# Kernel tuning notes

Hardware: AMD Instinct MI355X
Metric: run time of the kernel (lower is better)

Reference implementation:

```python
import jax, jax.numpy as jnp
import numpy as np
import math

B, NRES, RPR = 1, 384, 3
L = NRES * RPR          # 1152 rigids
CS, CZ = 256, 128
CH, H, PQ, PV = 16, 8, 8, 12


def _ln(x, scale, bias):
    mu = jnp.mean(x, axis=-1, keepdims=True)
    var = jnp.var(x, axis=-1, keepdims=True)
    return (x - mu) * jax.lax.rsqrt(var + 1e-5) * scale + bias


def _quat_to_rot(q):
    q = q / jnp.linalg.norm(q, axis=-1, keepdims=True)
    w, x, y, z = q[..., 0], q[..., 1], q[..., 2], q[..., 3]
    r = jnp.stack([
        1 - 2 * (y * y + z * z), 2 * (x * y - w * z), 2 * (x * z + w * y),
        2 * (x * y + w * z), 1 - 2 * (x * x + z * z), 2 * (y * z - w * x),
        2 * (x * z - w * y), 2 * (y * z + w * x), 1 - 2 * (x * x + y * y),
    ], axis=-1)
    return r.reshape(q.shape[:-1] + (3, 3))


def setup_inputs() -> dict:
    key = jax.random.key(0)
    ks = jax.random.split(key, 20)
    s = jax.random.normal(ks[0], (B, L, CS), jnp.float32)
    z = jax.random.normal(ks[1], (B, NRES, NRES, CZ), jnp.float32)
    rot = _quat_to_rot(jax.random.normal(ks[2], (B, L, 4), jnp.float32))
    trans = 10.0 * jax.random.normal(ks[3], (B, L, 3), jnp.float32)
    mask = jnp.ones((B, L), jnp.float32)
    rigid_to_res_idx = jnp.broadcast_to(jnp.arange(L, dtype=jnp.int32) // RPR, (B, L))
    w = lambda k, sh: 0.02 * jax.random.normal(k, sh, jnp.float32)
    return {
        "s": s, "z": z, "rot": rot, "trans": trans, "mask": mask,
        "ln_s_scale": jnp.ones((CS,), jnp.float32), "ln_s_bias": jnp.zeros((CS,), jnp.float32),
        "ln_z_scale": jnp.ones((CZ,), jnp.float32), "ln_z_bias": jnp.zeros((CZ,), jnp.float32),
        "w_q": w(ks[4], (CS, H * CH)), "w_k": w(ks[5], (CS, H * CH)), "w_v": w(ks[6], (CS, H * CH)),
        "w_qp": w(ks[7], (CS, H * PQ * 3)), "w_kp": w(ks[8], (CS, H * PQ * 3)), "w_vp": w(ks[9], (CS, H * PV * 3)),
        "w_b": w(ks[10], (CZ, H)),
        "head_weights": jnp.full((H,), 0.5413, jnp.float32),  # softplus^-1(1)
        "w_out": w(ks[11], (H * (CH + CZ + PV * 4), CS)),
        "b_out": jnp.zeros((CS,), jnp.float32),
        "rigid_to_res_idx": rigid_to_res_idx,
    }


def reference(s, z, rot, trans, mask, ln_s_scale, ln_s_bias, ln_z_scale, ln_z_bias,
              w_q, w_k, w_v, w_qp, w_kp, w_vp, w_b, head_weights, w_out, b_out,
              rigid_to_res_idx):
    b_, l_ = s.shape[0], s.shape[1]
    idx = rigid_to_res_idx[0]                       # [L] rigid -> residue, shared over batch
    s_ln = _ln(s, ln_s_scale, ln_s_bias)            # [B,L,CS]
    z_ln = _ln(z, ln_z_scale, ln_z_bias)            # [B,N,N,CZ]

    q = (s_ln @ w_q).reshape(b_, l_, H, CH)
    k = (s_ln @ w_k).reshape(b_, l_, H, CH)
    v = (s_ln @ w_v).reshape(b_, l_, H, CH)

    # local points, then rigid-transform to global frame: x_g = R x + t
    q_p = (s_ln @ w_qp).reshape(b_, l_, H, PQ, 3)
    k_p = (s_ln @ w_kp).reshape(b_, l_, H, PQ, 3)
    v_p = (s_ln @ w_vp).reshape(b_, l_, H, PV, 3)
    t5 = trans[:, :, None, None, :]
    q_g = jnp.einsum("blij,blhpj->blhpi", rot, q_p) + t5
    k_g = jnp.einsum("blij,blhpj->blhpi", rot, k_p) + t5
    v_g = jnp.einsum("blij,blhpj->blhpi", rot, v_p) + t5

    # scalar qk term
    a = jnp.einsum("blhc,bjhc->bhlj", q, k) * math.sqrt(1.0 / (3 * CH))
    # pair bias, broadcast residue-pair -> rigid-pair
    b_res = z_ln @ w_b                                # [B,N,N,H]
    b_full = b_res[:, idx][:, :, idx]                 # [B,L,L,H]
    a = a + math.sqrt(1.0 / 3) * jnp.transpose(b_full, (0, 3, 1, 2))
    # point-distance term: ||q-k||^2 = |q|^2 + |k|^2 - 2 q.k (summed over P,3)
    hw = jax.nn.softplus(head_weights) * math.sqrt(1.0 / (3 * (PQ * 9.0 / 2)))
    qq = jnp.sum(q_g * q_g, axis=(-1, -2)).transpose(0, 2, 1)   # [B,H,L]
    kk = jnp.sum(k_g * k_g, axis=(-1, -2)).transpose(0, 2, 1)
    qk = jnp.einsum("blhpc,bjhpc->bhlj", q_g, k_g)
    d2 = qq[:, :, :, None] + kk[:, :, None, :] - 2.0 * qk
    a = a - 0.5 * d2 * hw[None, :, None, None]
    a = a + (mask[:, None, None, :] - 1.0) * 1e9
    attn = jax.nn.softmax(a, axis=-1)                 # [B,H,L,L]

    o = jnp.einsum("bhlj,bjhc->blhc", attn, v)        # [B,L,H,CH]
    o_pt_g = jnp.einsum("bhlj,bjhpc->blhpc", attn, v_g)
    # back to local frame of query rigid: R^T (x - t)
    o_pt = jnp.einsum("blji,blhpj->blhpi", rot, o_pt_g - t5)
    o_pt_norm = jnp.sqrt(jnp.sum(o_pt * o_pt, axis=-1) + 1e-8)  # [B,L,H,PV]
    # pair output: sum attention over rigids belonging to each key residue
    attn_res = attn.reshape(b_, H, l_, NRES, RPR).sum(-1)       # [B,H,L,N]
    z_l = z_ln[:, idx]                                           # [B,L,N,CZ]
    o_pair = jnp.einsum("bhln,blnc->blhc", attn_res, z_l)        # [B,L,H,CZ]

    cat = jnp.concatenate(
        [o, o_pt.reshape(b_, l_, H, PV * 3), o_pt_norm, o_pair], axis=-1
    ).reshape(b_, l_, H * (CH + PV * 4 + CZ))
    return cat @ w_out + b_out                        # [B,L,CS]
```

## Files before the change

### kernel.cpp

```cpp
#include <hip/hip_runtime.h>
#include <hip/hip_bf16.h>

#define L 1152
#define NRES 384
#define CS 256
#define CZ 128
#define H 8
#define CH 16
#define PQ 8
#define PV 12
#define PSTR 1088

#define OFF_SLN  0L
#define OFF_PROJ 294912L
#define OFF_WPK  1548288L
#define OFF_QCAT 1826816L
#define OFF_KCAT 2232320L
#define OFF_VCAT 2637824L
#define OFF_BRES 3227648L
#define OFF_MURS 4407296L
#define OFF_ATTN 4702208L
#define OFF_CAT  15319040L
#define OFF_PCAT 17088512L
#define OFF_RSTAT 18268160L
#define OFF_PAV  18286592L
#define OFF_POP  21825536L
#define OFF_ARES 26544128L

__global__ __launch_bounds__(256) void k_ln_s(const float* s, const float* sc, const float* bi, float* sln){
  int l = blockIdx.x, t = threadIdx.x;
  __shared__ float red[CS];
  float x = s[(long)l*CS + t];
  red[t] = x; __syncthreads();
  for(int st=128; st>0; st>>=1){ if(t<st) red[t]+=red[t+st]; __syncthreads(); }
  float mu = red[0] * (1.f/CS); __syncthreads();
  float d = x - mu;
  red[t] = d*d; __syncthreads();
  for(int st=128; st>0; st>>=1){ if(t<st) red[t]+=red[t+st]; __syncthreads(); }
  float var = red[0]*(1.f/CS);
  sln[(long)l*CS + t] = d*rsqrtf(var + 1e-5f)*sc[t] + bi[t];
}

__global__ __launch_bounds__(256) void k_packw(const float* wq, const float* wk, const float* wv,
                        const float* wqp, const float* wkp, const float* wvp, float* wpack){
  int k = blockIdx.x, t = threadIdx.x;
  for(int c=t; c<PSTR; c+=256){
    float v;
    if(c<128)        v = wq [(long)k*128 + c];
    else if(c<256)   v = wk [(long)k*128 + c-128];
    else if(c<384)   v = wv [(long)k*128 + c-256];
    else if(c<576)   v = wqp[(long)k*192 + c-384];
    else if(c<768)   v = wkp[(long)k*192 + c-576];
    else if(c<1056)  v = wvp[(long)k*288 + c-768];
    else             v = 0.f;
    wpack[(long)k*PSTR + c] = v;
  }
}

__global__ __launch_bounds__(256) void k_proj(const float* sln, const float* wpack, float* proj){
  int l0 = blockIdx.x*64, c0 = blockIdx.y*64, t = threadIdx.x;
  __shared__ float a_s[32][68];
  __shared__ __align__(16) float w_s[32][68];
  int tr = t>>4, tc = t&15;
  float4 acc[4] = {{0,0,0,0},{0,0,0,0},{0,0,0,0},{0,0,0,0}};
  for(int kc=0; kc<8; kc++){
    int k0 = kc*32;
    {
      int row = t>>2, kk0 = (t&3)*8;
      const float4* src = (const float4*)(sln + (long)(l0+row)*256 + k0 + kk0);
      float4 v0 = src[0], v1 = src[1];
      a_s[kk0+0][row]=v0.x; a_s[kk0+1][row]=v0.y; a_s[kk0+2][row]=v0.z; a_s[kk0+3][row]=v0.w;
      a_s[kk0+4][row]=v1.x; a_s[kk0+5][row]=v1.y; a_s[kk0+6][row]=v1.z; a_s[kk0+7][row]=v1.w;
    }
    #pragma unroll
    for(int kk2=0; kk2<2; kk2++){
      int kk = (t>>4) + 16*kk2;
      *(float4*)&w_s[kk][(t&15)*4] = *(const float4*)(wpack + (long)(k0+kk)*PSTR + c0 + (t&15)*4);
    }
    __syncthreads();
    #pragma unroll 8
    for(int kk=0; kk<32; kk++){
      float4 a4 = *(const float4*)&a_s[kk][tr*4];
      float4 b4 = *(const float4*)&w_s[kk][tc*4];
      acc[0].x+=a4.x*b4.x; acc[0].y+=a4.x*b4.y; acc[0].z+=a4.x*b4.z; acc[0].w+=a4.x*b4.w;
      acc[1].x+=a4.y*b4.x; acc[1].y+=a4.y*b4.y; acc[1].z+=a4.y*b4.z; acc[1].w+=a4.y*b4.w;
      acc[2].x+=a4.z*b4.x; acc[2].y+=a4.z*b4.y; acc[2].z+=a4.z*b4.z; acc[2].w+=a4.z*b4.w;
      acc[3].x+=a4.w*b4.x; acc[3].y+=a4.w*b4.y; acc[3].z+=a4.w*b4.z; acc[3].w+=a4.w*b4.w;
    }
    __syncthreads();
  }
  #pragma unroll
  for(int r=0;r<4;r++)
    *(float4*)(proj + (long)(l0 + tr*4 + r)*PSTR + c0 + tc*4) = acc[r];
}

__global__ __launch_bounds__(256) void k_ln_z(const float* z, const float* sc, const float* bi,
                       const float* wb, float* murs, float* bres_t){
  int t = threadIdx.x;
  long rp0 = (long)blockIdx.x*32;
  int r = t>>3, part = t&7;
  long rp = rp0 + r;
  __shared__ __align__(16) float swb[8*132];
  __shared__ float SB[8][2];
  const float4* z4 = (const float4*)z;
  float4 x0 = z4[rp*32 + part*4 + 0];
  float4 x1 = z4[rp*32 + part*4 + 1];
  float4 x2 = z4[rp*32 + part*4 + 2];
  float4 x3 = z4[rp*32 + part*4 + 3];
  #pragma unroll
  for(int k2=0;k2<4;k2++){
    int e = t + k2*256; int h = e>>7, c = e&127;
    swb[h*132 + c] = sc[c]*wb[(long)c*8 + h];
  }
  __syncthreads();
  if(t < 64){
    int h = t>>3, seg = t&7;
    float S=0, Bv=0;
    #pragma unroll
    for(int i=0;i<16;i++){
      int c = seg*16+i;
      S  += swb[h*132+c];
      Bv += bi[c]*wb[(long)c*8 + h];
    }
    #pragma unroll
    for(int off=1;off<8;off<<=1){ S += __shfl_xor(S,off,64); Bv += __shfl_xor(Bv,off,64); }
    if(seg==0){ SB[h][0]=S; SB[h][1]=Bv; }
  }
  float s1 = x0.x+x0.y+x0.z+x0.w + x1.x+x1.y+x1.z+x1.w
           + x2.x+x2.y+x2.z+x2.w + x3.x+x3.y+x3.z+x3.w;
  float s2 = x0.x*x0.x+x0.y*x0.y+x0.z*x0.z+x0.w*x0.w
           + x1.x*x1.x+x1.y*x1.y+x1.z*x1.z+x1.w*x1.w
           + x2.x*x2.x+x2.y*x2.y+x2.z*x2.z+x2.w*x2.w
           + x3.x*x3.x+x3.y*x3.y+x3.z*x3.z+x3.w*x3.w;
  #pragma unroll
  for(int off=1;off<8;off<<=1){ s1 += __shfl_xor(s1,off,64); s2 += __shfl_xor(s2,off,64); }
  float mu = s1*(1.f/CZ);
  float var = s2*(1.f/CZ) - mu*mu;
  float rstd = rsqrtf(var + 1e-5f);
  if(part==0){ murs[rp*2]=mu; murs[rp*2+1]=rstd; }
  float acc[8];
  const float4* swb4 = (const float4*)swb;
  #pragma unroll
  for(int h=0;h<8;h++){
    float4 wa = swb4[h*33 + part*4 + 0];
    float4 wbv= swb4[h*33 + part*4 + 1];
    float4 wc = swb4[h*33 + part*4 + 2];
    float4 wd = swb4[h*33 + part*4 + 3];
    acc[h] = x0.x*wa.x + x0.y*wa.y + x0.z*wa.z + x0.w*wa.w
           + x1.x*wbv.x+ x1.y*wbv.y+ x1.z*wbv.z+ x1.w*wbv.w
           + x2.x*wc.x + x2.y*wc.y + x2.z*wc.z + x2.w*wc.w
           + x3.x*wd.x + x3.y*wd.y + x3.z*wd.z + x3.w*wd.w;
  }
  #pragma unroll
  for(int off=1;off<8;off<<=1){
    #pragma unroll
    for(int h=0;h<8;h++) acc[h] += __shfl_xor(acc[h],off,64);
  }
  __syncthreads();
  if(part==0){
    #pragma unroll
    for(int h=0;h<8;h++)
      bres_t[(long)h*147456 + rp] = rstd*(acc[h] - mu*SB[h][0]) + SB[h][1];
  }
}

__global__ __launch_bounds__(256) void k_rigid(const float* proj, const float* rot, const float* trans,
                        const float* mask, const float* hws,
                        float* qcat, float* kcat, float* vcat){
  int l = blockIdx.x, t = threadIdx.x;
  __shared__ float R[9], T[3], hwS[8], qgs[192], kgs[192];
  if(t<9) R[t]=rot[(long)l*9+t];
  if(t<3) T[t]=trans[(long)l*3+t];
  if(t>=16 && t<24) hwS[t-16] = log1pf(expf(hws[t-16]))*0.09622504486493764f;
  __syncthreads();
  const float* pr = proj + (long)l*PSTR;
  if(t<128){
    int h=t>>4, c=t&15;
    long base = ((long)h*L + l)*44;
    qcat[base + c] = 0.14433756729740643f * pr[t];
    kcat[base + c] = pr[128+t];
    vcat[((long)h*L + l)*64 + c] = pr[256+t];
  }
  if(t < 192){
    int h=t/24, m=t%24, p=m/3, i=m%3;
    float qa = R[i*3+0]*pr[384+h*24+p*3+0] + R[i*3+1]*pr[384+h*24+p*3+1]
             + R[i*3+2]*pr[384+h*24+p*3+2] + T[i];
    float ka = R[i*3+0]*pr[576+h*24+p*3+0] + R[i*3+1]*pr[576+h*24+p*3+1]
             + R[i*3+2]*pr[576+h*24+p*3+2] + T[i];
    qgs[t]=qa; kgs[t]=ka;
    long base = ((long)h*L + l)*44 + 16 + m;
    qcat[base] = hwS[h]*qa;
    kcat[base] = ka;
  }
  for(int it=t; it<288; it+=256){
    int h=it/36, m=it%36, p=m/3, i=m%3;
    float a = R[i*3+0]*pr[768+h*36+p*3+0] + R[i*3+1]*pr[768+h*36+p*3+1]
            + R[i*3+2]*pr[768+h*36+p*3+2] + T[i];
    vcat[((long)h*L + l)*64 + 16 + m] = a;
  }
  if(t < 96){
    int h=t/12, d=t%12;
    vcat[((long)h*L + l)*64 + 52 + d] = 0.f;
  }
  __syncthreads();
  if(t < 8){
    float qq=0, kk=0;
    #pragma unroll
    for(int m=0;m<24;m++){ qq += qgs[t*24+m]*qgs[t*24+m]; kk += kgs[t*24+m]*kgs[t*24+m]; }
    long base = ((long)t*L + l)*44;
    qcat[base + 40] = -0.5f*hwS[t]*qq;
    kcat[base + 40] = -0.5f*hwS[t]*kk + (mask[l]-1.f)*1e9f;
  }
}

__global__ __launch_bounds__(256) void k_scores(const float* qcat, const float* kcat,
                         const float* bres_t, const int* ridx, float* attn){
  int l0 = blockIdx.x*32, j0 = blockIdx.y*64, h = blockIdx.z;
  int t = threadIdx.x;
  __shared__ __align__(16) float q_s[32*44];
  __shared__ __align__(16) float k_s[64*44];
  __shared__ int rj_s[64];
  {
    const float* srcq = qcat + ((long)h*L + l0)*44;
    for(int i=t; i<32*44; i+=256) q_s[i]=srcq[i];
    const float* srck = kcat + ((long)h*L + j0)*44;
    for(int i=t; i<64*44; i+=256) k_s[i]=srck[i];
    if(t<64) rj_s[t]=ridx[j0+t];
  }
  __syncthreads();
  int a = t>>5;
  int b = t&31;
  float acc[4][2] = {{0,0},{0,0},{0,0},{0,0}};
  const float4* q4 = (const float4*)q_s;
  const float4* k4 = (const float4*)k_s;
  #pragma unroll
  for(int i=0;i<10;i++){
    float4 kA = k4[(long)b*11 + i];
    float4 kB = k4[(long)(b+32)*11 + i];
    #pragma unroll
    for(int r=0;r<4;r++){
      float4 qv = q4[(long)(a+8*r)*11 + i];
      acc[r][0] += qv.x*kA.x + qv.y*kA.y + qv.z*kA.z + qv.w*kA.w;
      acc[r][1] += qv.x*kB.x + qv.y*kB.y + qv.z*kB.z + qv.w*kB.w;
    }
  }
  float colc0 = k_s[b*44+40], colc1 = k_s[(b+32)*44+40];
  int rj0 = rj_s[b], rj1 = rj_s[b+32];
  const float* bbh = bres_t + (long)h*147456;
  #pragma unroll
  for(int r=0;r<4;r++){
    int row = a+8*r;
    float rowc = q_s[row*44+40];
    int rl = ridx[l0+row];
    const float* bb = bbh + (long)rl*NRES;
    float s0 = acc[r][0] + rowc + colc0 + 0.5773502691896258f*bb[rj0];
    float s1 = acc[r][1] + rowc + colc1 + 0.5773502691896258f*bb[rj1];
    float* arow = attn + ((long)h*L + l0+row)*L + j0;
    arow[b]    = s0;
    arow[b+32] = s1;
  }
}

__global__ __launch_bounds__(256) void k_rowstat(const float* attn, float* rowstat, float* ares){
  long row = (long)blockIdx.x*4 + (threadIdx.x>>6);
  int lane = threadIdx.x & 63;
  int w = threadIdx.x >> 6;
  __shared__ float es[4][1152];
  const float* p = attn + row*L;
  float v[18];
  float m=-1e30f;
  #pragma unroll
  for(int i=0;i<18;i++){ v[i]=p[lane + i*64]; m=fmaxf(m,v[i]); }
  #pragma unroll
  for(int off=1;off<64;off<<=1) m=fmaxf(m,__shfl_xor(m,off,64));
  float s=0;
  #pragma unroll
  for(int i=0;i<18;i++){ v[i]=__expf(v[i]-m); s+=v[i]; }
  #pragma unroll
  for(int off=1;off<64;off<<=1) s+=__shfl_xor(s,off,64);
  float inv = 1.f/s;
  if(lane==0){ rowstat[row*2]=m; rowstat[row*2+1]=inv; }
  #pragma unroll
  for(int i=0;i<18;i++) es[w][lane + i*64] = v[i]*inv;
  __syncthreads();
  #pragma unroll
  for(int q=0;q<6;q++){
    int n = lane + q*64;
    ares[row*NRES + n] = es[w][3*n] + es[w][3*n+1] + es[w][3*n+2];
  }
}

__global__ __launch_bounds__(256) void k_av(const float* attn, const float* vcat,
                     const float* rowstat, float* pav){
  int lb = blockIdx.x, h = blockIdx.y, sp = blockIdx.z, t = threadIdx.x;
  int l0 = lb*32;
  __shared__ float a_s[64][33];
  __shared__ __align__(16) float v_s[64][68];
  int lgrp = t>>4, dgrp = t&15;
  float4 acc0 = {0,0,0,0}, acc1 = {0,0,0,0};
  const float* abase = attn + ((long)h*L + l0)*L;
  int al = t>>3, jj0 = (t&7)*8;
  float mrow = rowstat[((long)h*L + l0 + al)*2];
  float irow = rowstat[((long)h*L + l0 + al)*2 + 1];
  for(int jc=sp*3; jc<sp*3+3; jc++){
    int j0 = jc*64;
    {
      const float4* src = (const float4*)(abase + (long)al*L + j0 + jj0);
      float4 p0 = src[0], p1 = src[1];
      a_s[jj0+0][al]=__expf(p0.x-mrow)*irow;
      a_s[jj0+1][al]=__expf(p0.y-mrow)*irow;
      a_s[jj0+2][al]=__expf(p0.z-mrow)*irow;
      a_s[jj0+3][al]=__expf(p0.w-mrow)*irow;
      a_s[jj0+4][al]=__expf(p1.x-mrow)*irow;
      a_s[jj0+5][al]=__expf(p1.y-mrow)*irow;
      a_s[jj0+6][al]=__expf(p1.z-mrow)*irow;
      a_s[jj0+7][al]=__expf(p1.w-mrow)*irow;
    }
    {
      int jj = t>>2, seg = t&3;
      const float4* src = (const float4*)(vcat + ((long)h*L + j0 + jj)*64 + seg*16);
      float4 q0=src[0], q1=src[1], q2=src[2], q3=src[3];
      float4* dst = (float4*)&v_s[jj][seg*16];
      dst[0]=q0; dst[1]=q1; dst[2]=q2; dst[3]=q3;
    }
    __syncthreads();
    #pragma unroll 8
    for(int jj=0; jj<64; jj++){
      float a0 = a_s[jj][lgrp*2], a1 = a_s[jj][lgrp*2+1];
      const float4 vv = *(const float4*)&v_s[jj][dgrp*4];
      acc0.x+=a0*vv.x; acc0.y+=a0*vv.y; acc0.z+=a0*vv.z; acc0.w+=a0*vv.w;
      acc1.x+=a1*vv.x; acc1.y+=a1*vv.y; acc1.z+=a1*vv.z; acc1.w+=a1*vv.w;
    }
    __syncthreads();
  }
  float* dst = pav + (((long)sp*H + h)*L + l0 + lgrp*2)*64 + dgrp*4;
  *(float4*)dst = acc0;
  *(float4*)(dst + 64) = acc1;
}

__global__ __launch_bounds__(256) void k_avred(const float* pav, const float* rot, const float* trans,
                        float* cat){
  int lb = blockIdx.x, h = blockIdx.y, t = threadIdx.x;
  int l0 = lb*32;
  __shared__ __align__(16) float fin_s[32][64];
  #pragma unroll
  for(int k=0;k<2;k++){
    int fi = t + k*256;
    int l = fi>>4, c4 = fi&15;
    long base = (((long)h)*L + l0 + l)*64 + c4*4;
    float4 r = {0,0,0,0};
    #pragma unroll
    for(int p=0;p<6;p++){
      float4 a = *(const float4*)(pav + (long)p*589824 + base);
      r.x+=a.x; r.y+=a.y; r.z+=a.z; r.w+=a.w;
    }
    *(float4*)&fin_s[l][c4*4] = r;
  }
  __syncthreads();
  for(int it=t; it<32*16; it+=256){
    int l=it>>4, c=it&15;
    cat[(long)(l0+l)*1536 + h*192 + c] = fin_s[l][c];
  }
  for(int it=t; it<32*12; it+=256){
    int l=it/12, p=it%12;
    long gl = l0+l;
    float og0 = fin_s[l][16+p*3+0]-trans[gl*3+0];
    float og1 = fin_s[l][16+p*3+1]-trans[gl*3+1];
    float og2 = fin_s[l][16+p*3+2]-trans[gl*3+2];
    float* crow = cat + gl*1536 + h*192;
    float nrm=0;
    #pragma unroll
    for(int i=0;i<3;i++){
      float v = rot[gl*9+0+i]*og0 + rot[gl*9+3+i]*og1 + rot[gl*9+6+i]*og2;
      crow[16+p*3+i]=v; nrm+=v*v;
    }
    crow[52+p]=sqrtf(nrm+1e-8f);
  }
}

#define OPAIR_STEP(Z0,Z1,Z2,Z3,NB) { \
    float4 a0 = *(const float4*)&ar[0][th][NB]; \
    float4 a1 = *(const float4*)&ar[1][th][NB]; \
    float4 a2 = *(const float4*)&ar[2][th][NB]; \
    acc[0][0] += a0.x*Z0.x + a0.y*Z1.x + a0.z*Z2.x + a0.w*Z3.x; \
    acc[0][1] += a0.x*Z0.y + a0.y*Z1.y + a0.z*Z2.y + a0.w*Z3.y; \
    acc[0][2] += a0.x*Z0.z + a0.y*Z1.z + a0.z*Z2.z + a0.w*Z3.z; \
    acc[0][3] += a0.x*Z0.w + a0.y*Z1.w + a0.z*Z2.w + a0.w*Z3.w; \
    acc[1][0] += a1.x*Z0.x + a1.y*Z1.x + a1.z*Z2.x + a1.w*Z3.x; \
    acc[1][1] += a1.x*Z0.y + a1.y*Z1.y + a1.z*Z2.y + a1.w*Z3.y; \
    acc[1][2] += a1.x*Z0.z + a1.y*Z1.z + a1.z*Z2.z + a1.w*Z3.z; \
    acc[1][3] += a1.x*Z0.w + a1.y*Z1.w + a1.z*Z2.w + a1.w*Z3.w; \
    acc[2][0] += a2.x*Z0.x + a2.y*Z1.x + a2.z*Z2.x + a2.w*Z3.x; \
    acc[2][1] += a2.x*Z0.y + a2.y*Z1.y + a2.z*Z2.y + a2.w*Z3.y; \
    acc[2][2] += a2.x*Z0.z + a2.y*Z1.z + a2.z*Z2.z + a2.w*Z3.z; \
    acc[2][3] += a2.x*Z0.w + a2.y*Z1.w + a2.z*Z2.w + a2.w*Z3.w; }

__global__ __launch_bounds__(256) void k_opair(const float* ares, const float* z, const float* murs,
                        const float* sc, const int* ridx, float* po){
  int r=blockIdx.x, sp=blockIdx.y, t=threadIdx.x;
  __shared__ __align__(16) float ar[3][H][96];
  __shared__ __align__(16) float mrs[96*2];
  __shared__ float S1s[24];
  int rl = ridx[r*3];
  int n0 = sp*96;
  int tc = t&31, th = t>>5;
  const float* zbase = z + ((long)(rl*NRES + n0))*CZ + tc*4;
  float4 zc0 = *(const float4*)(zbase + 0L*CZ);
  float4 zc1 = *(const float4*)(zbase + 1L*CZ);
  float4 zc2 = *(const float4*)(zbase + 2L*CZ);
  float4 zc3 = *(const float4*)(zbase + 3L*CZ);
  for(int i=t;i<192;i+=256) mrs[i]=murs[((long)rl*NRES + n0)*2 + i];
  __syncthreads();
  for(int it=t; it<3*H*96; it+=256){
    int lo = it/(H*96);
    int rem = it - lo*(H*96);
    int h = rem/96, n = rem - h*96;
    ar[lo][h][n] = ares[((long)h*L + r*3+lo)*NRES + n0 + n] * mrs[n*2+1];
  }
  __syncthreads();
  if(t<192){
    int row=t>>3, seg=t&7;
    const float* arr = ((const float*)ar) + row*96 + seg*12;
    const float* mur = mrs + seg*24;
    float s1=0;
    #pragma unroll
    for(int q2=0;q2<12;q2++) s1 += arr[q2]*mur[q2*2];
    s1 += __shfl_xor(s1,1,64); s1 += __shfl_xor(s1,2,64); s1 += __shfl_xor(s1,4,64);
    if(seg==0) S1s[row]=s1;
  }
  __syncthreads();
  float acc[3][4]={};
  for(int nb=0; nb<88; nb+=8){
    float4 zn0 = *(const float4*)(zbase + (long)(nb+4)*CZ);
    float4 zn1 = *(const float4*)(zbase + (long)(nb+5)*CZ);
    float4 zn2 = *(const float4*)(zbase + (long)(nb+6)*CZ);
    float4 zn3 = *(const float4*)(zbase + (long)(nb+7)*CZ);
    OPAIR_STEP(zc0,zc1,zc2,zc3, nb);
    zc0 = *(const float4*)(zbase + (long)(nb+ 8)*CZ);
    zc1 = *(const float4*)(zbase + (long)(nb+ 9)*CZ);
    zc2 = *(const float4*)(zbase + (long)(nb+10)*CZ);
    zc3 = *(const float4*)(zbase + (long)(nb+11)*CZ);
    OPAIR_STEP(zn0,zn1,zn2,zn3, nb+4);
  }
  {
    float4 zn0 = *(const float4*)(zbase + 92L*CZ);
    float4 zn1 = *(const float4*)(zbase + 93L*CZ);
    float4 zn2 = *(const float4*)(zbase + 94L*CZ);
    float4 zn3 = *(const float4*)(zbase + 95L*CZ);
    OPAIR_STEP(zc0,zc1,zc2,zc3, 88);
    OPAIR_STEP(zn0,zn1,zn2,zn3, 92);
  }
  float4 sc4 = *(const float4*)(sc + tc*4);
  #pragma unroll
  for(int lo=0;lo<3;lo++){
    float s1v = S1s[lo*8+th];
    float4 o = { sc4.x*(acc[lo][0]-s1v), sc4.y*(acc[lo][1]-s1v),
                 sc4.z*(acc[lo][2]-s1v), sc4.w*(acc[lo][3]-s1v) };
    *(float4*)(po + ((long)sp*L + (long)(r*3+lo))*1024 + th*128 + tc*4) = o;
  }
}

__global__ __launch_bounds__(256) void k_opred(const float* po, const float* bi, float* cat){
  int i = blockIdx.x*256 + threadIdx.x;
  const float4* p = (const float4*)po;
  float4 a = p[i], b = p[i + 294912], c = p[i + 589824], d = p[i + 884736];
  int l = i>>8, rem = i&255;
  int h = rem>>5, c4 = rem&31;
  float4 bv = ((const float4*)bi)[c4];
  float4 r = {a.x+b.x+c.x+d.x+bv.x, a.y+b.y+c.y+d.y+bv.y,
              a.z+b.z+c.z+d.z+bv.z, a.w+b.w+c.w+d.w+bv.w};
  ((float4*)cat)[(long)l*384 + h*48 + 16 + c4] = r;
}

__global__ __launch_bounds__(256) void k_final(const float* cat, const float* wout, float* pcat){
  int l0 = blockIdx.x*32, c0 = blockIdx.y*32, kp = blockIdx.z, t = threadIdx.x;
  __shared__ float a_s[64][33];
  __shared__ __align__(16) float w_s[64][36];
  int tr = t>>3, tc = t&7;
  float4 acc = {0,0,0,0};
  for(int kc=0; kc<6; kc++){
    int k0 = kp*384 + kc*64;
    {
      int row = t>>3, kk0 = (t&7)*8;
      const float4* src = (const float4*)(cat + (long)(l0+row)*1536 + k0 + kk0);
      float4 v0 = src[0], v1 = src[1];
      a_s[kk0+0][row]=v0.x; a_s[kk0+1][row]=v0.y; a_s[kk0+2][row]=v0.z; a_s[kk0+3][row]=v0.w;
      a_s[kk0+4][row]=v1.x; a_s[kk0+5][row]=v1.y; a_s[kk0+6][row]=v1.z; a_s[kk0+7][row]=v1.w;
    }
    #pragma unroll
    for(int kk2=0; kk2<2; kk2++){
      int kk = (t>>3) + 32*kk2;
      *(float4*)&w_s[kk][(t&7)*4] = *(const float4*)(wout + (long)(k0+kk)*256 + c0 + (t&7)*4);
    }
    __syncthreads();
    #pragma unroll 8
    for(int kk=0; kk<64; kk++){
      float a0 = a_s[kk][tr];
      float4 b4 = *(const float4*)&w_s[kk][tc*4];
      acc.x+=a0*b4.x; acc.y+=a0*b4.y; acc.z+=a0*b4.z; acc.w+=a0*b4.w;
    }
    __syncthreads();
  }
  *(float4*)(pcat + ((long)kp*L + l0+tr)*256 + c0 + tc*4) = acc;
}

__global__ __launch_bounds__(256) void k_redout(const float* pcat, const float* bout, float* out){
  int i = blockIdx.x*256 + threadIdx.x;
  const float4* p = (const float4*)pcat;
  float4 a = p[i], b = p[i+73728], c = p[i+147456], d = p[i+221184];
  float4 bv = ((const float4*)bout)[i&63];
  float4 r;
  r.x = a.x+b.x+c.x+d.x+bv.x;
  r.y = a.y+b.y+c.y+d.y+bv.y;
  r.z = a.z+b.z+c.z+d.z+bv.z;
  r.w = a.w+b.w+c.w+d.w+bv.w;
  ((float4*)out)[i] = r;
}

extern "C" void kernel_launch(void* const* d_in, const int* in_sizes, int n_in,
                              void* d_out, int out_size, void* d_ws, size_t ws_size,
                              hipStream_t stream) {
  const float* s      = (const float*)d_in[0];
  const float* z      = (const float*)d_in[1];
  const float* rot    = (const float*)d_in[2];
  const float* trans  = (const float*)d_in[3];
  const float* mask   = (const float*)d_in[4];
  const float* lnss   = (const float*)d_in[5];
  const float* lnsb   = (const float*)d_in[6];
  const float* lnzs   = (const float*)d_in[7];
  const float* lnzb   = (const float*)d_in[8];
  const float* wq     = (const float*)d_in[9];
  const float* wk     = (const float*)d_in[10];
  const float* wv     = (const float*)d_in[11];
  const float* wqp    = (const float*)d_in[12];
  const float* wkp    = (const float*)d_in[13];
  const float* wvp    = (const float*)d_in[14];
  const float* wb     = (const float*)d_in[15];
  const float* hws    = (const float*)d_in[16];
  const float* wout   = (const float*)d_in[17];
  const float* bout   = (const float*)d_in[18];
  const int*  ridx    = (const int*)d_in[19];

  float* ws  = (float*)d_ws;
  float* out = (float*)d_out;

  float* sln  = ws + OFF_SLN;
  float* proj = ws + OFF_PROJ;
  float* wpk  = ws + OFF_WPK;
  float* qcat = ws + OFF_QCAT;
  float* kcat = ws + OFF_KCAT;
  float* vcat = ws + OFF_VCAT;
  float* bres = ws + OFF_BRES;
  float* murs = ws + OFF_MURS;
  float* attn = ws + OFF_ATTN;
  float* cat  = ws + OFF_CAT;
  float* pcat = ws + OFF_PCAT;
  float* rstat= ws + OFF_RSTAT;
  float* pav  = ws + OFF_PAV;
  float* po   = ws + OFF_POP;
  float* ares = ws + OFF_ARES;

  k_packw<<<dim3(256), dim3(256), 0, stream>>>(wq, wk, wv, wqp, wkp, wvp, wpk);
  k_ln_s<<<dim3(L), dim3(CS), 0, stream>>>(s, lnss, lnsb, sln);
  k_proj<<<dim3(18,17), dim3(256), 0, stream>>>(sln, wpk, proj);
  k_ln_z<<<dim3(NRES*NRES/32), dim3(256), 0, stream>>>(z, lnzs, lnzb, wb, murs, bres);
  k_rigid<<<dim3(L), dim3(256), 0, stream>>>(proj, rot, trans, mask, hws, qcat, kcat, vcat);
  k_scores<<<dim3(L/32, L/64, H), dim3(256), 0, stream>>>(qcat, kcat, bres, ridx, attn);
  k_rowstat<<<dim3(H*L/4), dim3(256), 0, stream>>>(attn, rstat, ares);
  k_av<<<dim3(L/32, H, 6), dim3(256), 0, stream>>>(attn, vcat, rstat, pav);
  k_avred<<<dim3(L/32, H), dim3(256), 0, stream>>>(pav, rot, trans, cat);
  k_opair<<<dim3(NRES, 4), dim3(256), 0, stream>>>(ares, z, murs, lnzs, ridx, po);
  k_opred<<<dim3(1152), dim3(256), 0, stream>>>(po, lnzb, cat);
  k_final<<<dim3(36,8,4), dim3(256), 0, stream>>>(cat, wout, pcat);
  k_redout<<<dim3(288), dim3(256), 0, stream>>>(pcat, bout, out);
}
```

Measured before the change: 322.7 us.

## Merge prologue and epilogue kernels and store normalized softmax in rowstat

Three independent preprocessing kernels (weight pack, s layernorm, z layernorm plus pair bias) are merged into one launch by splitting on block index. The avred and opred reductions are merged the same way into a single k_post launch. k_rowstat now writes the normalized probabilities back into the attention buffer, so k_av no longer recomputes exp and the rowstat buffer is removed. This trades launch overhead and duplicated exp work for an extra full write of the 8x1152x1152 attention matrix.

```diff
diff --git a/kernel.cpp b/kernel.cpp
--- a/kernel.cpp
+++ b/kernel.cpp
@@ -22,38 +22,112 @@
 #define OFF_ATTN 4702208L
 #define OFF_CAT  15319040L
 #define OFF_PCAT 17088512L
-#define OFF_RSTAT 18268160L
 #define OFF_PAV  18286592L
 #define OFF_POP  21825536L
 #define OFF_ARES 26544128L
 
-__global__ __launch_bounds__(256) void k_ln_s(const float* s, const float* sc, const float* bi, float* sln){
-  int l = blockIdx.x, t = threadIdx.x;
-  __shared__ float red[CS];
-  float x = s[(long)l*CS + t];
-  red[t] = x; __syncthreads();
-  for(int st=128; st>0; st>>=1){ if(t<st) red[t]+=red[t+st]; __syncthreads(); }
-  float mu = red[0] * (1.f/CS); __syncthreads();
-  float d = x - mu;
-  red[t] = d*d; __syncthreads();
-  for(int st=128; st>0; st>>=1){ if(t<st) red[t]+=red[t+st]; __syncthreads(); }
-  float var = red[0]*(1.f/CS);
-  sln[(long)l*CS + t] = d*rsqrtf(var + 1e-5f)*sc[t] + bi[t];
-}
-
-__global__ __launch_bounds__(256) void k_packw(const float* wq, const float* wk, const float* wv,
-                        const float* wqp, const float* wkp, const float* wvp, float* wpack){
-  int k = blockIdx.x, t = threadIdx.x;
-  for(int c=t; c<PSTR; c+=256){
-    float v;
-    if(c<128)        v = wq [(long)k*128 + c];
-    else if(c<256)   v = wk [(long)k*128 + c-128];
-    else if(c<384)   v = wv [(long)k*128 + c-256];
-    else if(c<576)   v = wqp[(long)k*192 + c-384];
-    else if(c<768)   v = wkp[(long)k*192 + c-576];
-    else if(c<1056)  v = wvp[(long)k*288 + c-768];
-    else             v = 0.f;
-    wpack[(long)k*PSTR + c] = v;
+__global__ __launch_bounds__(256) void k_pre(
+    const float* wq, const float* wk, const float* wv,
+    const float* wqp, const float* wkp, const float* wvp, float* wpack,
+    const float* s, const float* lnss, const float* lnsb, float* sln,
+    const float* z, const float* lnzs, const float* lnzb,
+    const float* wb, float* murs, float* bres_t){
+  int bx = blockIdx.x, t = threadIdx.x;
+  if(bx < 256){
+    int k = bx;
+    for(int c=t; c<PSTR; c+=256){
+      float v;
+      if(c<128)        v = wq [(long)k*128 + c];
+      else if(c<256)   v = wk [(long)k*128 + c-128];
+      else if(c<384)   v = wv [(long)k*128 + c-256];
+      else if(c<576)   v = wqp[(long)k*192 + c-384];
+      else if(c<768)   v = wkp[(long)k*192 + c-576];
+      else if(c<1056)  v = wvp[(long)k*288 + c-768];
+      else             v = 0.f;
+      wpack[(long)k*PSTR + c] = v;
+    }
+    return;
+  }
+  if(bx < 256 + L){
+    int l = bx - 256;
+    __shared__ float red[CS];
+    float x = s[(long)l*CS + t];
+    red[t] = x; __syncthreads();
+    for(int st=128; st>0; st>>=1){ if(t<st) red[t]+=red[t+st]; __syncthreads(); }
+    float mu = red[0] * (1.f/CS); __syncthreads();
+    float d = x - mu;
+    red[t] = d*d; __syncthreads();
+    for(int st=128; st>0; st>>=1){ if(t<st) red[t]+=red[t+st]; __syncthreads(); }
+    float var = red[0]*(1.f/CS);
+    sln[(long)l*CS + t] = d*rsqrtf(var + 1e-5f)*lnss[t] + lnsb[t];
+    return;
+  }
+  {
+    long rp0 = (long)(bx - 256 - L)*32;
+    int r = t>>3, part = t&7;
+    long rp = rp0 + r;
+    __shared__ __align__(16) float swb[8*132];
+    __shared__ float SB[8][2];
+    const float4* z4 = (const float4*)z;
+    float4 x0 = z4[rp*32 + part*4 + 0];
+    float4 x1 = z4[rp*32 + part*4 + 1];
+    float4 x2 = z4[rp*32 + part*4 + 2];
+    float4 x3 = z4[rp*32 + part*4 + 3];
+    #pragma unroll
+    for(int k2=0;k2<4;k2++){
+      int e = t + k2*256; int h = e>>7, c = e&127;
+      swb[h*132 + c] = lnzs[c]*wb[(long)c*8 + h];
+    }
+    __syncthreads();
+    if(t < 64){
+      int h = t>>3, seg = t&7;
+      float S=0, Bv=0;
+      #pragma unroll
+      for(int i=0;i<16;i++){
+        int c = seg*16+i;
+        S  += swb[h*132+c];
+        Bv += lnzb[c]*wb[(long)c*8 + h];
+      }
+      #pragma unroll
+      for(int off=1;off<8;off<<=1){ S += __shfl_xor(S,off,64); Bv += __shfl_xor(Bv,off,64); }
+      if(seg==0){ SB[h][0]=S; SB[h][1]=Bv; }
+    }
+    float s1 = x0.x+x0.y+x0.z+x0.w + x1.x+x1.y+x1.z+x1.w
+             + x2.x+x2.y+x2.z+x2.w + x3.x+x3.y+x3.z+x3.w;
+    float s2 = x0.x*x0.x+x0.y*x0.y+x0.z*x0.z+x0.w*x0.w
+             + x1.x*x1.x+x1.y*x1.y+x1.z*x1.z+x1.w*x1.w
+             + x2.x*x2.x+x2.y*x2.y+x2.z*x2.z+x2.w*x2.w
+             + x3.x*x3.x+x3.y*x3.y+x3.z*x3.z+x3.w*x3.w;
+    #pragma unroll
+    for(int off=1;off<8;off<<=1){ s1 += __shfl_xor(s1,off,64); s2 += __shfl_xor(s2,off,64); }
+    float mu = s1*(1.f/CZ);
+    float var = s2*(1.f/CZ) - mu*mu;
+    float rstd = rsqrtf(var + 1e-5f);
+    if(part==0){ murs[rp*2]=mu; murs[rp*2+1]=rstd; }
+    float acc[8];
+    const float4* swb4 = (const float4*)swb;
+    #pragma unroll
+    for(int h=0;h<8;h++){
+      float4 wa = swb4[h*33 + part*4 + 0];
+      float4 wbv= swb4[h*33 + part*4 + 1];
+      float4 wc = swb4[h*33 + part*4 + 2];
+      float4 wd = swb4[h*33 + part*4 + 3];
+      acc[h] = x0.x*wa.x + x0.y*wa.y + x0.z*wa.z + x0.w*wa.w
+             + x1.x*wbv.x+ x1.y*wbv.y+ x1.z*wbv.z+ x1.w*wbv.w
+             + x2.x*wc.x + x2.y*wc.y + x2.z*wc.z + x2.w*wc.w
+             + x3.x*wd.x + x3.y*wd.y + x3.z*wd.z + x3.w*wd.w;
+    }
+    #pragma unroll
+    for(int off=1;off<8;off<<=1){
+      #pragma unroll
+      for(int h=0;h<8;h++) acc[h] += __shfl_xor(acc[h],off,64);
+    }
+    __syncthreads();
+    if(part==0){
+      #pragma unroll
+      for(int h=0;h<8;h++)
+        bres_t[(long)h*147456 + rp] = rstd*(acc[h] - mu*SB[h][0]) + SB[h][1];
+    }
   }
 }
 
@@ -94,76 +168,6 @@
     *(float4*)(proj + (long)(l0 + tr*4 + r)*PSTR + c0 + tc*4) = acc[r];
 }
 
-__global__ __launch_bounds__(256) void k_ln_z(const float* z, const float* sc, const float* bi,
-                       const float* wb, float* murs, float* bres_t){
-  int t = threadIdx.x;
-  long rp0 = (long)blockIdx.x*32;
-  int r = t>>3, part = t&7;
-  long rp = rp0 + r;
-  __shared__ __align__(16) float swb[8*132];
-  __shared__ float SB[8][2];
-  const float4* z4 = (const float4*)z;
-  float4 x0 = z4[rp*32 + part*4 + 0];
-  float4 x1 = z4[rp*32 + part*4 + 1];
-  float4 x2 = z4[rp*32 + part*4 + 2];
-  float4 x3 = z4[rp*32 + part*4 + 3];
-  #pragma unroll
-  for(int k2=0;k2<4;k2++){
-    int e = t + k2*256; int h = e>>7, c = e&127;
-    swb[h*132 + c] = sc[c]*wb[(long)c*8 + h];
-  }
-  __syncthreads();
-  if(t < 64){
-    int h = t>>3, seg = t&7;
-    float S=0, Bv=0;
-    #pragma unroll
-    for(int i=0;i<16;i++){
-      int c = seg*16+i;
-      S  += swb[h*132+c];
-      Bv += bi[c]*wb[(long)c*8 + h];
-    }
-    #pragma unroll
-    for(int off=1;off<8;off<<=1){ S += __shfl_xor(S,off,64); Bv += __shfl_xor(Bv,off,64); }
-    if(seg==0){ SB[h][0]=S; SB[h][1]=Bv; }
-  }
-  float s1 = x0.x+x0.y+x0.z+x0.w + x1.x+x1.y+x1.z+x1.w
-           + x2.x+x2.y+x2.z+x2.w + x3.x+x3.y+x3.z+x3.w;
-  float s2 = x0.x*x0.x+x0.y*x0.y+x0.z*x0.z+x0.w*x0.w
-           + x1.x*x1.x+x1.y*x1.y+x1.z*x1.z+x1.w*x1.w
-           + x2.x*x2.x+x2.y*x2.y+x2.z*x2.z+x2.w*x2.w
-           + x3.x*x3.x+x3.y*x3.y+x3.z*x3.z+x3.w*x3.w;
-  #pragma unroll
-  for(int off=1;off<8;off<<=1){ s1 += __shfl_xor(s1,off,64); s2 += __shfl_xor(s2,off,64); }
-  float mu = s1*(1.f/CZ);
-  float var = s2*(1.f/CZ) - mu*mu;
-  float rstd = rsqrtf(var + 1e-5f);
-  if(part==0){ murs[rp*2]=mu; murs[rp*2+1]=rstd; }
-  float acc[8];
-  const float4* swb4 = (const float4*)swb;
-  #pragma unroll
-  for(int h=0;h<8;h++){
-    float4 wa = swb4[h*33 + part*4 + 0];
-    float4 wbv= swb4[h*33 + part*4 + 1];
-    float4 wc = swb4[h*33 + part*4 + 2];
-    float4 wd = swb4[h*33 + part*4 + 3];
-    acc[h] = x0.x*wa.x + x0.y*wa.y + x0.z*wa.z + x0.w*wa.w
-           + x1.x*wbv.x+ x1.y*wbv.y+ x1.z*wbv.z+ x1.w*wbv.w
-           + x2.x*wc.x + x2.y*wc.y + x2.z*wc.z + x2.w*wc.w
-           + x3.x*wd.x + x3.y*wd.y + x3.z*wd.z + x3.w*wd.w;
-  }
-  #pragma unroll
-  for(int off=1;off<8;off<<=1){
-    #pragma unroll
-    for(int h=0;h<8;h++) acc[h] += __shfl_xor(acc[h],off,64);
-  }
-  __syncthreads();
-  if(part==0){
-    #pragma unroll
-    for(int h=0;h<8;h++)
-      bres_t[(long)h*147456 + rp] = rstd*(acc[h] - mu*SB[h][0]) + SB[h][1];
-  }
-}
-
 __global__ __launch_bounds__(256) void k_rigid(const float* proj, const float* rot, const float* trans,
                         const float* mask, const float* hws,
                         float* qcat, float* kcat, float* vcat){
@@ -261,12 +265,12 @@
   }
 }
 
-__global__ __launch_bounds__(256) void k_rowstat(const float* attn, float* rowstat, float* ares){
+__global__ __launch_bounds__(256) void k_rowstat(float* attn, float* ares){
   long row = (long)blockIdx.x*4 + (threadIdx.x>>6);
   int lane = threadIdx.x & 63;
   int w = threadIdx.x >> 6;
   __shared__ float es[4][1152];
-  const float* p = attn + row*L;
+  float* p = attn + row*L;
   float v[18];
   float m=-1e30f;
   #pragma unroll
@@ -279,9 +283,12 @@
   #pragma unroll
   for(int off=1;off<64;off<<=1) s+=__shfl_xor(s,off,64);
   float inv = 1.f/s;
-  if(lane==0){ rowstat[row*2]=m; rowstat[row*2+1]=inv; }
-  #pragma unroll
-  for(int i=0;i<18;i++) es[w][lane + i*64] = v[i]*inv;
+  #pragma unroll
+  for(int i=0;i<18;i++){
+    float pv = v[i]*inv;
+    p[lane + i*64] = pv;
+    es[w][lane + i*64] = pv;
+  }
   __syncthreads();
   #pragma unroll
   for(int q=0;q<6;q++){
@@ -290,8 +297,7 @@
   }
 }
 
-__global__ __launch_bounds__(256) void k_av(const float* attn, const float* vcat,
-                     const float* rowstat, float* pav){
+__global__ __launch_bounds__(256) void k_av(const float* attn, const float* vcat, float* pav){
   int lb = blockIdx.x, h = blockIdx.y, sp = blockIdx.z, t = threadIdx.x;
   int l0 = lb*32;
   __shared__ float a_s[64][33];
@@ -300,21 +306,15 @@
   float4 acc0 = {0,0,0,0}, acc1 = {0,0,0,0};
   const float* abase = attn + ((long)h*L + l0)*L;
   int al = t>>3, jj0 = (t&7)*8;
-  float mrow = rowstat[((long)h*L + l0 + al)*2];
-  float irow = rowstat[((long)h*L + l0 + al)*2 + 1];
   for(int jc=sp*3; jc<sp*3+3; jc++){
     int j0 = jc*64;
     {
       const float4* src = (const float4*)(abase + (long)al*L + j0 + jj0);
       float4 p0 = src[0], p1 = src[1];
-      a_s[jj0+0][al]=__expf(p0.x-mrow)*irow;
-      a_s[jj0+1][al]=__expf(p0.y-mrow)*irow;
-      a_s[jj0+2][al]=__expf(p0.z-mrow)*irow;
-      a_s[jj0+3][al]=__expf(p0.w-mrow)*irow;
-      a_s[jj0+4][al]=__expf(p1.x-mrow)*irow;
-      a_s[jj0+5][al]=__expf(p1.y-mrow)*irow;
-      a_s[jj0+6][al]=__expf(p1.z-mrow)*irow;
-      a_s[jj0+7][al]=__expf(p1.w-mrow)*irow;
+      a_s[jj0+0][al]=p0.x; a_s[jj0+1][al]=p0.y;
+      a_s[jj0+2][al]=p0.z; a_s[jj0+3][al]=p0.w;
+      a_s[jj0+4][al]=p1.x; a_s[jj0+5][al]=p1.y;
+      a_s[jj0+6][al]=p1.z; a_s[jj0+7][al]=p1.w;
     }
     {
       int jj = t>>2, seg = t&3;
@@ -336,46 +336,6 @@
   float* dst = pav + (((long)sp*H + h)*L + l0 + lgrp*2)*64 + dgrp*4;
   *(float4*)dst = acc0;
   *(float4*)(dst + 64) = acc1;
-}
-
-__global__ __launch_bounds__(256) void k_avred(const float* pav, const float* rot, const float* trans,
-                        float* cat){
-  int lb = blockIdx.x, h = blockIdx.y, t = threadIdx.x;
-  int l0 = lb*32;
-  __shared__ __align__(16) float fin_s[32][64];
-  #pragma unroll
-  for(int k=0;k<2;k++){
-    int fi = t + k*256;
-    int l = fi>>4, c4 = fi&15;
-    long base = (((long)h)*L + l0 + l)*64 + c4*4;
-    float4 r = {0,0,0,0};
-    #pragma unroll
-    for(int p=0;p<6;p++){
-      float4 a = *(const float4*)(pav + (long)p*589824 + base);
-      r.x+=a.x; r.y+=a.y; r.z+=a.z; r.w+=a.w;
-    }
-    *(float4*)&fin_s[l][c4*4] = r;
-  }
-  __syncthreads();
-  for(int it=t; it<32*16; it+=256){
-    int l=it>>4, c=it&15;
-    cat[(long)(l0+l)*1536 + h*192 + c] = fin_s[l][c];
-  }
-  for(int it=t; it<32*12; it+=256){
-    int l=it/12, p=it%12;
-    long gl = l0+l;
-    float og0 = fin_s[l][16+p*3+0]-trans[gl*3+0];
-    float og1 = fin_s[l][16+p*3+1]-trans[gl*3+1];
-    float og2 = fin_s[l][16+p*3+2]-trans[gl*3+2];
-    float* crow = cat + gl*1536 + h*192;
-    float nrm=0;
-    #pragma unroll
-    for(int i=0;i<3;i++){
-      float v = rot[gl*9+0+i]*og0 + rot[gl*9+3+i]*og1 + rot[gl*9+6+i]*og2;
-      crow[16+p*3+i]=v; nrm+=v*v;
-    }
-    crow[52+p]=sqrtf(nrm+1e-8f);
-  }
 }
 
 #define OPAIR_STEP(Z0,Z1,Z2,Z3,NB) { \
@@ -460,16 +420,59 @@
   }
 }
 
-__global__ __launch_bounds__(256) void k_opred(const float* po, const float* bi, float* cat){
-  int i = blockIdx.x*256 + threadIdx.x;
-  const float4* p = (const float4*)po;
-  float4 a = p[i], b = p[i + 294912], c = p[i + 589824], d = p[i + 884736];
-  int l = i>>8, rem = i&255;
-  int h = rem>>5, c4 = rem&31;
-  float4 bv = ((const float4*)bi)[c4];
-  float4 r = {a.x+b.x+c.x+d.x+bv.x, a.y+b.y+c.y+d.y+bv.y,
-              a.z+b.z+c.z+d.z+bv.z, a.w+b.w+c.w+d.w+bv.w};
-  ((float4*)cat)[(long)l*384 + h*48 + 16 + c4] = r;
+__global__ __launch_bounds__(256) void k_post(const float* pav, const float* rot, const float* trans,
+                        const float* po, const float* bi, float* cat){
+  int bx = blockIdx.x, t = threadIdx.x;
+  if(bx < 288){
+    int lb = bx % 36, h = bx / 36;
+    int l0 = lb*32;
+    __shared__ __align__(16) float fin_s[32][64];
+    #pragma unroll
+    for(int k=0;k<2;k++){
+      int fi = t + k*256;
+      int l = fi>>4, c4 = fi&15;
+      long base = (((long)h)*L + l0 + l)*64 + c4*4;
+      float4 r = {0,0,0,0};
+      #pragma unroll
+      for(int p=0;p<6;p++){
+        float4 a = *(const float4*)(pav + (long)p*589824 + base);
+        r.x+=a.x; r.y+=a.y; r.z+=a.z; r.w+=a.w;
+      }
+      *(float4*)&fin_s[l][c4*4] = r;
+    }
+    __syncthreads();
+    for(int it=t; it<32*16; it+=256){
+      int l=it>>4, c=it&15;
+      cat[(long)(l0+l)*1536 + h*192 + c] = fin_s[l][c];
+    }
+    for(int it=t; it<32*12; it+=256){
+      int l=it/12, p=it%12;
+      long gl = l0+l;
+      float og0 = fin_s[l][16+p*3+0]-trans[gl*3+0];
+      float og1 = fin_s[l][16+p*3+1]-trans[gl*3+1];
+      float og2 = fin_s[l][16+p*3+2]-trans[gl*3+2];
+      float* crow = cat + gl*1536 + h*192;
+      float nrm=0;
+      #pragma unroll
+      for(int i=0;i<3;i++){
+        float v = rot[gl*9+0+i]*og0 + rot[gl*9+3+i]*og1 + rot[gl*9+6+i]*og2;
+        crow[16+p*3+i]=v; nrm+=v*v;
+      }
+      crow[52+p]=sqrtf(nrm+1e-8f);
+    }
+    return;
+  }
+  {
+    int i = (bx-288)*256 + t;
+    const float4* p = (const float4*)po;
+    float4 a = p[i], b = p[i + 294912], c = p[i + 589824], d = p[i + 884736];
+    int l = i>>8, rem = i&255;
+    int h = rem>>5, c4 = rem&31;
+    float4 bv = ((const float4*)bi)[c4];
+    float4 r = {a.x+b.x+c.x+d.x+bv.x, a.y+b.y+c.y+d.y+bv.y,
+                a.z+b.z+c.z+d.z+bv.z, a.w+b.w+c.w+d.w+bv.w};
+    ((float4*)cat)[(long)l*384 + h*48 + 16 + c4] = r;
+  }
 }
 
 __global__ __launch_bounds__(256) void k_final(const float* cat, const float* wout, float* pcat){
@@ -555,22 +558,21 @@
   float* attn = ws + OFF_ATTN;
   float* cat  = ws + OFF_CAT;
   float* pcat = ws + OFF_PCAT;
-  float* rstat= ws + OFF_RSTAT;
   float* pav  = ws + OFF_PAV;
   float* po   = ws + OFF_POP;
   float* ares = ws + OFF_ARES;
 
-  k_packw<<<dim3(256), dim3(256), 0, stream>>>(wq, wk, wv, wqp, wkp, wvp, wpk);
-  k_ln_s<<<dim3(L), dim3(CS), 0, stream>>>(s, lnss, lnsb, sln);
+  k_pre<<<dim3(256 + L + NRES*NRES/32), dim3(256), 0, stream>>>(
+      wq, wk, wv, wqp, wkp, wvp, wpk,
+      s, lnss, lnsb, sln,
+      z, lnzs, lnzb, wb, murs, bres);
   k_proj<<<dim3(18,17), dim3(256), 0, stream>>>(sln, wpk, proj);
-  k_ln_z<<<dim3(NRES*NRES/32), dim3(256), 0, stream>>>(z, lnzs, lnzb, wb, murs, bres);
   k_rigid<<<dim3(L), dim3(256), 0, stream>>>(proj, rot, trans, mask, hws, qcat, kcat, vcat);
   k_scores<<<dim3(L/32, L/64, H), dim3(256), 0, stream>>>(qcat, kcat, bres, ridx, attn);
-  k_rowstat<<<dim3(H*L/4), dim3(256), 0, stream>>>(attn, rstat, ares);
-  k_av<<<dim3(L/32, H, 6), dim3(256), 0, stream>>>(attn, vcat, rstat, pav);
-  k_avred<<<dim3(L/32, H), dim3(256), 0, stream>>>(pav, rot, trans, cat);
+  k_rowstat<<<dim3(H*L/4), dim3(256), 0, stream>>>(attn, ares);
+  k_av<<<dim3(L/32, H, 6), dim3(256), 0, stream>>>(attn, vcat, pav);
   k_opair<<<dim3(NRES, 4), dim3(256), 0, stream>>>(ares, z, murs, lnzs, ridx, po);
-  k_opred<<<dim3(1152), dim3(256), 0, stream>>>(po, lnzb, cat);
+  k_post<<<dim3(288 + 1152), dim3(256), 0, stream>>>(pav, rot, trans, po, lnzb, cat);
   k_final<<<dim3(36,8,4), dim3(256), 0, stream>>>(cat, wout, pcat);
   k_redout<<<dim3(288), dim3(256), 0, stream>>>(pcat, bout, out);
 }
```

Result: no change. 320.2 us (-0.8%).
